# Optimization experiments

Hardware: AMD Instinct MI355X
Metric: run time of the kernel (lower is better)

## Reference

```python
import jax, jax.numpy as jnp
import numpy as np

TEMPERATURE = 0.07

def setup_inputs() -> dict:
    key = jax.random.key(0)
    k1, k2 = jax.random.split(key)
    B, D = 16384, 64
    return {
        "embeddings_a": jax.random.normal(k1, (B, D), dtype=jnp.float32),
        "embeddings_b": jax.random.normal(k2, (B, D), dtype=jnp.float32),
    }

def reference(embeddings_a, embeddings_b):
    # cosine similarity: L2-normalize rows, then dot product, scaled by temperature
    a = embeddings_a / jnp.linalg.norm(embeddings_a, axis=1, keepdims=True)
    b = embeddings_b / jnp.linalg.norm(embeddings_b, axis=1, keepdims=True)
    sim = jnp.einsum('id,jd->ij', a, b) / TEMPERATURE  # [B, B]
    # Default mask: positives on the diagonal, negatives everywhere else.
    # Per-row cross-entropy over [pos, negs] with target 0 is exactly
    # logsumexp(row) - sim[i, i]  (pos appears once among the logits).
    losses = jax.scipy.special.logsumexp(sim, axis=1) - jnp.diagonal(sim)
    return jnp.mean(losses)  # reduction='mean'
```

## Files before the change

### kernel.cpp

```cpp
#include <hip/hip_runtime.h>
#include <math.h>


#define NROWS 16384
#define DIM 64
#define INV_T 14.285714285714286f
#define LOG2E 1.44269504088896340736f
#define LN2   0.69314718055994530942f
#define SCALE (INV_T * LOG2E * 8388608.0f)
#define BIASF 1064990828.0f

#define JC     32
#define JPC    (NROWS / JC)
#define NTILES (JPC / 16)
#define TT     4
#define WR     (TT * 16)
#define NWAVE  8
#define BROWS  (NWAVE * WR)
#define ROWB   (DIM * 2)
#define LDSB   (JPC * ROWB)
#define TILB   (16 * ROWB)

typedef __attribute__((ext_vector_type(8))) short bf16x8;
typedef __attribute__((ext_vector_type(4))) float f32x4;

static __device__ __forceinline__ unsigned short f2bf(float f) {
    unsigned int u = __float_as_uint(f);
    unsigned int r = (u + 0x7fffu + ((u >> 16) & 1u)) >> 16;
    return (unsigned short)r;
}

__global__ __launch_bounds__(256) void nrm_bf16_kernel(
        const float* __restrict__ A, const float* __restrict__ B,
        unsigned short* __restrict__ Ab, unsigned short* __restrict__ Bb) {
    int wid  = (blockIdx.x * 256 + threadIdx.x) >> 6;
    int lane = threadIdx.x & 63;
    const float* in;
    unsigned short* out;
    float scale;
    int row;
    if (wid < NROWS) { in = A; out = Ab; scale = SCALE; row = wid; }
    else             { in = B; out = Bb; scale = 1.0f;  row = wid - NROWS; }
    float x  = in[row * DIM + lane];
    float ss = x * x;
    #pragma unroll
    for (int m = 32; m >= 1; m >>= 1) ss += __shfl_xor(ss, m, 64);
    out[row * DIM + lane] = f2bf(x * rsqrtf(ss) * scale);
}

__global__ __launch_bounds__(NWAVE * 64) void simexp_kernel(
        const unsigned short* __restrict__ Ab,
        const unsigned short* __restrict__ Bb,
        float* __restrict__ partials) {
    __shared__ __align__(1024) unsigned char lds[LDSB];
    const int lane = threadIdx.x & 63;
    const int wid  = threadIdx.x >> 6;
    const int jc   = blockIdx.x & (JC - 1);
    const int rb   = blockIdx.x / JC;
    const int i0   = rb * BROWS + wid * WR;
    const int lr   = lane & 15;
    const int lk   = lane >> 4;

    const unsigned char* gB = (const unsigned char*)Bb + (size_t)jc * JPC * ROWB;
    const int perm = ((lane >> 3) << 7) | ((((lane & 7) ^ (lane >> 3))) << 4);
    #pragma unroll
    for (int i = 0; i < LDSB / 1024 / NWAVE; ++i) {
        const int off = (wid * (LDSB / 1024 / NWAVE) + i) * 1024;
        __builtin_amdgcn_global_load_lds(
            (const __attribute__((address_space(1))) void*)(gB + off + perm),
            (__attribute__((address_space(3))) void*)(&lds[off]),
            16, 0, 0);
    }

    bf16x8 a[TT][2];
    #pragma unroll
    for (int t = 0; t < TT; ++t) {
        const unsigned short* ap = Ab + (size_t)(i0 + t * 16 + lr) * DIM + lk * 8;
        a[t][0] = *(const bf16x8*)(ap);
        a[t][1] = *(const bf16x8*)(ap + 32);
    }

    float es[TT][4];
    #pragma unroll
    for (int t = 0; t < TT; ++t)
        #pragma unroll
        for (int r = 0; r < 4; ++r) es[t][r] = 0.0f;

    __builtin_amdgcn_s_waitcnt(0x0f70);
    __syncthreads();

    const unsigned char* lp0 = &lds[lr * ROWB + (((lk    ) ^ (lr & 7)) << 4)];
    const unsigned char* lp1 = &lds[lr * ROWB + (((lk ^ 4) ^ (lr & 7)) << 4)];

    const f32x4 bias = {BIASF, BIASF, BIASF, BIASF};

    bf16x8 c0 = *(const bf16x8*)(lp0);
    bf16x8 c1 = *(const bf16x8*)(lp1);
    f32x4 accp[TT];
    #pragma unroll
    for (int t = 0; t < TT; ++t) {
        accp[t] = __builtin_amdgcn_mfma_f32_16x16x32_bf16(a[t][0], c0, bias, 0, 0, 0);
        accp[t] = __builtin_amdgcn_mfma_f32_16x16x32_bf16(a[t][1], c1, accp[t], 0, 0, 0);
    }

    for (int jt = 1; jt < NTILES; ++jt) {
        bf16x8 n0 = *(const bf16x8*)(lp0 + jt * TILB);
        bf16x8 n1 = *(const bf16x8*)(lp1 + jt * TILB);
        #pragma unroll
        for (int t = 0; t < TT; ++t)
            #pragma unroll
            for (int r = 0; r < 4; ++r)
                es[t][r] += __int_as_float((int)accp[t][r]);
        #pragma unroll
        for (int t = 0; t < TT; ++t) {
            accp[t] = __builtin_amdgcn_mfma_f32_16x16x32_bf16(a[t][0], n0, bias, 0, 0, 0);
            accp[t] = __builtin_amdgcn_mfma_f32_16x16x32_bf16(a[t][1], n1, accp[t], 0, 0, 0);
        }
    }
    #pragma unroll
    for (int t = 0; t < TT; ++t)
        #pragma unroll
        for (int r = 0; r < 4; ++r)
            es[t][r] += __int_as_float((int)accp[t][r]);

    #pragma unroll
    for (int t = 0; t < TT; ++t)
        #pragma unroll
        for (int r = 0; r < 4; ++r) {
            float v = es[t][r];
            v += __shfl_xor(v, 1, 64);
            v += __shfl_xor(v, 2, 64);
            v += __shfl_xor(v, 4, 64);
            v += __shfl_xor(v, 8, 64);
            es[t][r] = v;
        }

    if (lr == 0) {
        float* pout = partials + (size_t)jc * NROWS + i0;
        #pragma unroll
        for (int t = 0; t < TT; ++t) {
            f32x4 v = {es[t][0], es[t][1], es[t][2], es[t][3]};
            *(f32x4*)(pout + t * 16 + lk * 4) = v;
        }
    }
}

__global__ __launch_bounds__(256) void rowloss_kernel(
        const float* __restrict__ A, const float* __restrict__ B,
        const float* __restrict__ partials, float* __restrict__ rowloss) {
    int row  = (blockIdx.x * 256 + threadIdx.x) >> 6;
    int lane = threadIdx.x & 63;
    float a = A[row * DIM + lane];
    float b = B[row * DIM + lane];
    float saa = a * a, sbb = b * b, sab = a * b;
    float S = (lane < JC) ? partials[(size_t)lane * NROWS + row] : 0.0f;
    #pragma unroll
    for (int m = 32; m >= 1; m >>= 1) {
        saa += __shfl_xor(saa, m, 64);
        sbb += __shfl_xor(sbb, m, 64);
        sab += __shfl_xor(sab, m, 64);
        S   += __shfl_xor(S,   m, 64);
    }
    if (lane == 0) {
        float diag = sab * rsqrtf(saa * sbb);
        rowloss[row] = LN2 * __builtin_amdgcn_logf(S) - diag * INV_T;
    }
}

__global__ __launch_bounds__(1024) void mean_kernel(
        const float* __restrict__ rowloss, float* __restrict__ out) {
    float s = 0.f;
    for (int idx = threadIdx.x; idx < NROWS; idx += 1024) s += rowloss[idx];
    __shared__ float red[16];
    #pragma unroll
    for (int m = 32; m >= 1; m >>= 1) s += __shfl_xor(s, m, 64);
    if ((threadIdx.x & 63) == 0) red[threadIdx.x >> 6] = s;
    __syncthreads();
    if (threadIdx.x < 16) {
        float t = red[threadIdx.x];
        #pragma unroll
        for (int m = 8; m >= 1; m >>= 1) t += __shfl_xor(t, m, 16);
        if (threadIdx.x == 0) out[0] = t * (1.0f / NROWS);
    }
}

extern "C" void kernel_launch(void* const* d_in, const int* in_sizes, int n_in,
                              void* d_out, int out_size, void* d_ws, size_t ws_size,
                              hipStream_t stream) {
    const float* A  = (const float*)d_in[0];
    const float* Bm = (const float*)d_in[1];
    float* out = (float*)d_out;

    unsigned short* Ab = (unsigned short*)d_ws;
    unsigned short* Bb = Ab + (size_t)NROWS * DIM;
    float* partials    = (float*)(Bb + (size_t)NROWS * DIM);
    float* rowloss     = partials + (size_t)JC * NROWS;

    nrm_bf16_kernel<<<2 * NROWS / 4, 256, 0, stream>>>(A, Bm, Ab, Bb);
    simexp_kernel<<<JC * (NROWS / BROWS), NWAVE * 64, 0, stream>>>(Ab, Bb, partials);
    rowloss_kernel<<<NROWS / 4, 256, 0, stream>>>(A, Bm, partials, rowloss);
    mean_kernel<<<1, 1024, 0, stream>>>(rowloss, out);
}
```

Before: 57.29 us.

## Compute diagonal in normalize kernel, simplify row loss, double waves per block

```diff
diff --git a/kernel.cpp b/kernel.cpp
--- a/kernel.cpp
+++ b/kernel.cpp
@@ -15,7 +15,7 @@
 #define NTILES (JPC / 16)
 #define TT     4
 #define WR     (TT * 16)
-#define NWAVE  8
+#define NWAVE  16
 #define BROWS  (NWAVE * WR)
 #define ROWB   (DIM * 2)
 #define LDSB   (JPC * ROWB)
@@ -32,20 +32,22 @@
 
 __global__ __launch_bounds__(256) void nrm_bf16_kernel(
         const float* __restrict__ A, const float* __restrict__ B,
-        unsigned short* __restrict__ Ab, unsigned short* __restrict__ Bb) {
-    int wid  = (blockIdx.x * 256 + threadIdx.x) >> 6;
+        unsigned short* __restrict__ Ab, unsigned short* __restrict__ Bb,
+        float* __restrict__ diag) {
+    int row  = (blockIdx.x * 256 + threadIdx.x) >> 6;
     int lane = threadIdx.x & 63;
-    const float* in;
-    unsigned short* out;
-    float scale;
-    int row;
-    if (wid < NROWS) { in = A; out = Ab; scale = SCALE; row = wid; }
-    else             { in = B; out = Bb; scale = 1.0f;  row = wid - NROWS; }
-    float x  = in[row * DIM + lane];
-    float ss = x * x;
+    float xa = A[row * DIM + lane];
+    float xb = B[row * DIM + lane];
+    float saa = xa * xa, sbb = xb * xb, sab = xa * xb;
     #pragma unroll
-    for (int m = 32; m >= 1; m >>= 1) ss += __shfl_xor(ss, m, 64);
-    out[row * DIM + lane] = f2bf(x * rsqrtf(ss) * scale);
+    for (int m = 32; m >= 1; m >>= 1) {
+        saa += __shfl_xor(saa, m, 64);
+        sbb += __shfl_xor(sbb, m, 64);
+        sab += __shfl_xor(sab, m, 64);
+    }
+    Ab[row * DIM + lane] = f2bf(xa * rsqrtf(saa) * SCALE);
+    Bb[row * DIM + lane] = f2bf(xb * rsqrtf(sbb));
+    if (lane == 0) diag[row] = sab * rsqrtf(saa * sbb) * INV_T;
 }
 
 __global__ __launch_bounds__(NWAVE * 64) void simexp_kernel(
@@ -146,25 +148,13 @@
 }
 
 __global__ __launch_bounds__(256) void rowloss_kernel(
-        const float* __restrict__ A, const float* __restrict__ B,
-        const float* __restrict__ partials, float* __restrict__ rowloss) {
-    int row  = (blockIdx.x * 256 + threadIdx.x) >> 6;
-    int lane = threadIdx.x & 63;
-    float a = A[row * DIM + lane];
-    float b = B[row * DIM + lane];
-    float saa = a * a, sbb = b * b, sab = a * b;
-    float S = (lane < JC) ? partials[(size_t)lane * NROWS + row] : 0.0f;
+        const float* __restrict__ partials, const float* __restrict__ diag,
+        float* __restrict__ rowloss) {
+    int row = blockIdx.x * 256 + threadIdx.x;
+    float S = 0.0f;
     #pragma unroll
-    for (int m = 32; m >= 1; m >>= 1) {
-        saa += __shfl_xor(saa, m, 64);
-        sbb += __shfl_xor(sbb, m, 64);
-        sab += __shfl_xor(sab, m, 64);
-        S   += __shfl_xor(S,   m, 64);
-    }
-    if (lane == 0) {
-        float diag = sab * rsqrtf(saa * sbb);
-        rowloss[row] = LN2 * __builtin_amdgcn_logf(S) - diag * INV_T;
-    }
+    for (int c = 0; c < JC; ++c) S += partials[(size_t)c * NROWS + row];
+    rowloss[row] = LN2 * __builtin_amdgcn_logf(S) - diag[row];
 }
 
 __global__ __launch_bounds__(1024) void mean_kernel(
@@ -195,9 +185,10 @@
     unsigned short* Bb = Ab + (size_t)NROWS * DIM;
     float* partials    = (float*)(Bb + (size_t)NROWS * DIM);
     float* rowloss     = partials + (size_t)JC * NROWS;
+    float* diag        = rowloss + NROWS;
 
-    nrm_bf16_kernel<<<2 * NROWS / 4, 256, 0, stream>>>(A, Bm, Ab, Bb);
+    nrm_bf16_kernel<<<NROWS / 4, 256, 0, stream>>>(A, Bm, Ab, Bb, diag);
     simexp_kernel<<<JC * (NROWS / BROWS), NWAVE * 64, 0, stream>>>(Ab, Bb, partials);
-    rowloss_kernel<<<NROWS / 4, 256, 0, stream>>>(A, Bm, partials, rowloss);
+    rowloss_kernel<<<NROWS / 256, 256, 0, stream>>>(partials, diag, rowloss);
     mean_kernel<<<1, 1024, 0, stream>>>(rowloss, out);
 }
```

After: 56.60 us. No clear change (-1.2%).
